# Kernel tuning notes

Measured on AMD Instinct MI355X. Metric: run time of the kernel, lower is better.

## Reference

```python
import jax, jax.numpy as jnp
import numpy as np

B, L, W = 64, 20, 48
D = W * W           # 2304, MoE input/output size (image_width**2)
E = 4               # num_experts
HID = 2 * D         # expert hidden size
K = 1               # top_k
LOSS_COEF = 1e-2


def _cv_squared(x):
    # torch: x.var() (unbiased) / (x.mean()**2 + eps)
    eps = 1e-10
    return jnp.var(x, ddof=1) / (jnp.mean(x) ** 2 + eps)


def _moe(x, w_gate, w1, b1, w2, b2):
    # Noisy top-k gating, inference path (train=False => clean logits, no noise).
    logits = x @ w_gate                                   # [B, E]
    top_logits, top_idx = jax.lax.top_k(logits, K + 1)    # min(k+1, E)
    topk_gates = jax.nn.softmax(top_logits[:, :K], axis=-1)
    gates = jnp.zeros_like(logits).at[
        jnp.arange(x.shape[0])[:, None], top_idx[:, :K]
    ].set(topk_gates)                                     # [B, E] sparse gates
    importance = gates.sum(0)
    load = (gates > 0).sum(0).astype(x.dtype)             # _gates_to_load
    aux = LOSS_COEF * (_cv_squared(importance) + _cv_squared(load))
    # Dense expert compute weighted by gates (same math as dispatch/combine).
    h = jax.nn.relu(jnp.einsum('bd,edh->beh', x, w1) + b1)      # [B,E,HID]
    y = jnp.einsum('beh,ehd->bed', h, w2) + b2                  # [B,E,D]
    out = jnp.einsum('be,bed->bd', gates, y)                    # [B,D]
    return out, aux


def _conv3d(x, w, b, pad):
    y = jax.lax.conv_general_dilated(
        x, w, window_strides=(1, 1, 1), padding=pad,
        dimension_numbers=('NCDHW', 'OIDHW', 'NCDHW'))
    return y + b[None, :, None, None, None]


def _forward(input, conv1_w, conv1_b, conv2_w, conv2_b,
             t_gate, t_w1, t_b1, t_w2, t_b2,
             a_gate, a_w1, a_b1, a_w2, a_b2,
             q_gate, q_w1, q_b1, q_w2, q_b2,
             enc_w, enc_b, dec_w, dec_b):
    x = jnp.transpose(input, (0, 2, 1, 3, 4))                   # [B,1,L,H,W]
    x = jax.nn.relu(_conv3d(x, conv1_w, conv1_b, ((1, 1), (1, 1), (1, 1))))
    x = jax.nn.relu(_conv3d(x, conv2_w, conv2_b, ((0, 0), (1, 1), (1, 1))))  # [B,1,1,H,W]
    xf = x.reshape(x.shape[0], -1)                              # [B, D]
    transform, l1 = _moe(xf, t_gate, t_w1, t_b1, t_w2, t_b2)
    add, l2 = _moe(xf, a_gate, a_w1, a_b1, a_w2, a_b2)
    quad, l3 = _moe(xf, q_gate, q_w1, q_b1, q_w2, q_b2)
    s = input.shape                                             # [B,L,1,H,W]
    transform = transform.reshape(s[0], 1, s[2], s[3], s[4])
    add = add.reshape(s[0], 1, s[2], s[3], s[4])
    quad = quad.reshape(s[0], 1, s[2], s[3], s[4])
    out = input * input * quad + input * transform + add        # [B,L,1,H,W]
    # encoder = Linear(D,D)+ReLU, decoder = Linear(D,D) over flattened H*W
    of = out.reshape(s[0], s[1], D)
    of = jax.nn.relu(of @ enc_w + enc_b)
    of = of @ dec_w + dec_b
    of = jax.nn.sigmoid(of)
    return of.reshape(s), l1 + l2 + l3


def setup_inputs() -> dict:
    key = jax.random.key(0)
    ks = jax.random.split(key, 32)
    sc = 0.02
    inp = {
        'input': jax.random.normal(ks[0], (B, L, 1, W, W), jnp.float32),
        'conv1_w': jax.random.normal(ks[1], (10, 1, 3, 3, 3), jnp.float32) * sc,
        'conv1_b': jnp.zeros((10,), jnp.float32),
        'conv2_w': jax.random.normal(ks[2], (1, 10, L, 3, 3), jnp.float32) * sc,
        'conv2_b': jnp.zeros((1,), jnp.float32),
        'enc_w': jax.random.normal(ks[3], (D, D), jnp.float32) * sc,
        'enc_b': jnp.zeros((D,), jnp.float32),
        'dec_w': jax.random.normal(ks[4], (D, D), jnp.float32) * sc,
        'dec_b': jnp.zeros((D,), jnp.float32),
    }
    for i, p in enumerate(['t', 'a', 'q']):
        k0, k1, k2 = jax.random.split(ks[5 + i], 3)
        inp[p + '_gate'] = jnp.zeros((D, E), jnp.float32) + jax.random.normal(k0, (D, E), jnp.float32) * sc
        inp[p + '_w1'] = jax.random.normal(k1, (E, D, HID), jnp.float32) * sc
        inp[p + '_b1'] = jnp.zeros((E, HID), jnp.float32)
        inp[p + '_w2'] = jax.random.normal(k2, (E, HID, D), jnp.float32) * sc
        inp[p + '_b2'] = jnp.zeros((E, D), jnp.float32)
    return inp


def reference(input, conv1_w, conv1_b, conv2_w, conv2_b,
              t_gate, t_w1, t_b1, t_w2, t_b2,
              a_gate, a_w1, a_b1, a_w2, a_b2,
              q_gate, q_w1, q_b1, q_w2, q_b2,
              enc_w, enc_b, dec_w, dec_b):
    return _forward(input, conv1_w, conv1_b, conv2_w, conv2_b,
                    t_gate, t_w1, t_b1, t_w2, t_b2,
                    a_gate, a_w1, a_b1, a_w2, a_b2,
                    q_gate, q_w1, q_b1, q_w2, q_b2,
                    enc_w, enc_b, dec_w, dec_b)
```

## Files before the change

### kernel.cpp

```cpp
#include <hip/hip_runtime.h>
#include <stdint.h>

#define NB 64
#define NL 20
#define ND 2304
#define NE 4
#define NH 4608
#define NM 1280

typedef float f32x4 __attribute__((ext_vector_type(4)));
typedef __bf16 bf16x8 __attribute__((ext_vector_type(8)));
typedef unsigned short u16;
typedef u16 u16x4 __attribute__((ext_vector_type(4)));
typedef unsigned int u32;
typedef u32 u32x4 __attribute__((ext_vector_type(4)));

__device__ __forceinline__ u16 f2bf(float f) {
  u32 u = __builtin_bit_cast(u32, f);
  u += 0x7fffu + ((u >> 16) & 1u);
  return (u16)(u >> 16);
}

__device__ __forceinline__ void gl_lds16(const void* g, void* l) {
  __builtin_amdgcn_global_load_lds(
      (const __attribute__((address_space(1))) void*)g,
      (__attribute__((address_space(3))) void*)l, 16, 0, 0);
}

#define OFF_XF    147456
#define OFF_H     294912
#define OFF_Y     1179648
#define OFF_AUX   1622016
#define OFF_CNT   1622020
#define OFF_ROWS  1622032
#define OFF_OFB   1622240
#define OFF_H1B   3096800
#define OFF_ENCWB 4571360
#define OFF_DECWB 7225568
#define OFF_XC    9879776
#define OFF_P     10322144

__global__ __launch_bounds__(256) void k_conv(
    const float* __restrict__ in, const float* __restrict__ w1,
    const float* __restrict__ b1, const float* __restrict__ w2,
    float* __restrict__ xfp) {
  __shared__ float insl[3][20][50];
  __shared__ float c1[2][18][50];
  __shared__ float w1s[270];
  __shared__ float w2s[90];
  __shared__ float b1s[10];
  const int d = blockIdx.x, b = blockIdx.y, h = blockIdx.z, t = threadIdx.x;
  const int gy0 = h * 16;
  for (int i = t; i < 270; i += 256) w1s[i] = w1[i];
  for (int i = t; i < 90; i += 256) w2s[i] = w2[(size_t)((i / 9) * 20 + d) * 9 + (i % 9)];
  if (t < 10) b1s[t] = b1[t];
  for (int i = t; i < 3000; i += 256) {
    int s = i / 1000, rr = (i % 1000) / 50, cc = i % 50;
    int gd = d - 1 + s, gy = gy0 - 2 + rr, gx = cc - 1;
    float v = 0.f;
    if (gd >= 0 && gd < NL && (unsigned)gy < 48u && (unsigned)gx < 48u)
      v = in[((size_t)b * NL + gd) * ND + gy * 48 + gx];
    insl[s][rr][cc] = v;
  }
  for (int i = t; i < 1800; i += 256) ((float*)c1)[i] = 0.f;
  float s2[4] = {0.f, 0.f, 0.f, 0.f};
  const int y1 = t / 12, x0 = (t % 12) * 4;
  __syncthreads();
  for (int pc = 0; pc < 5; ++pc) {
    if (t < 216) {
      const int gr = gy0 - 1 + y1;
      if ((unsigned)gr < 48u) {
        float a0[4], a1[4];
        const float bb0 = b1s[2 * pc], bb1 = b1s[2 * pc + 1];
#pragma unroll
        for (int xq = 0; xq < 4; ++xq) { a0[xq] = bb0; a1[xq] = bb1; }
#pragma unroll
        for (int kd = 0; kd < 3; ++kd)
#pragma unroll
          for (int ky = 0; ky < 3; ++ky) {
            float v[6];
#pragma unroll
            for (int i = 0; i < 6; ++i) v[i] = insl[kd][y1 + ky][x0 + i];
            const float* wa = &w1s[(2 * pc) * 27 + kd * 9 + ky * 3];
            const float* wb = wa + 27;
#pragma unroll
            for (int xq = 0; xq < 4; ++xq) {
              a0[xq] += v[xq] * wa[0] + v[xq + 1] * wa[1] + v[xq + 2] * wa[2];
              a1[xq] += v[xq] * wb[0] + v[xq + 1] * wb[1] + v[xq + 2] * wb[2];
            }
          }
#pragma unroll
        for (int xq = 0; xq < 4; ++xq) {
          c1[0][y1][x0 + 1 + xq] = fmaxf(a0[xq], 0.f);
          c1[1][y1][x0 + 1 + xq] = fmaxf(a1[xq], 0.f);
        }
      }
    }
    __syncthreads();
    if (t < 192) {
#pragma unroll
      for (int cc = 0; cc < 2; ++cc) {
#pragma unroll
        for (int ky = 0; ky < 3; ++ky) {
          float v[6];
#pragma unroll
          for (int i = 0; i < 6; ++i) v[i] = c1[cc][y1 + ky][x0 + i];
          const float* wr = &w2s[(2 * pc + cc) * 9 + ky * 3];
#pragma unroll
          for (int xq = 0; xq < 4; ++xq)
            s2[xq] += v[xq] * wr[0] + v[xq + 1] * wr[1] + v[xq + 2] * wr[2];
        }
      }
    }
    __syncthreads();
  }
  if (t < 192) {
    f32x4 o = {s2[0], s2[1], s2[2], s2[3]};
    *(f32x4*)(xfp + ((size_t)d * NB + b) * ND + (gy0 + y1) * 48 + x0) = o;
  }
}

__global__ __launch_bounds__(256) void k_bias_relu(
    const float* __restrict__ xfp, const float* __restrict__ c2b, float* __restrict__ xf) {
  const size_t i = (size_t)blockIdx.x * 256 + threadIdx.x;
  float s = c2b[0];
#pragma unroll
  for (int d = 0; d < NL; ++d) s += xfp[(size_t)d * (NB * ND) + i];
  xf[i] = fmaxf(s, 0.f);
}

__global__ __launch_bounds__(256) void k_gate(
    const float* __restrict__ xf,
    const float* __restrict__ g0, const float* __restrict__ g1, const float* __restrict__ g2,
    float* __restrict__ aux, int* __restrict__ cnt, int* __restrict__ rows) {
  const int p = blockIdx.x, t = threadIdx.x;
  const float* __restrict__ g = (p == 0) ? g0 : ((p == 1) ? g1 : g2);
  __shared__ float lg[64][4];
  __shared__ int lidx[64];
  __shared__ int lcnt[4];
  if (t < 4) lcnt[t] = 0;
  const int wv = t >> 6, l = t & 63;
  for (int b0 = 0; b0 < 64; b0 += 4) {
    int bb = b0 + wv;
    f32x4 acc = {0.f, 0.f, 0.f, 0.f};
    const float* xr = xf + (size_t)bb * ND + l * 36;
    const float* gr = g + (size_t)l * 36 * 4;
#pragma unroll
    for (int i4 = 0; i4 < 9; ++i4) {
      f32x4 xv = *(const f32x4*)(xr + i4 * 4);
#pragma unroll
      for (int qq = 0; qq < 4; ++qq) {
        f32x4 gv = *(const f32x4*)(gr + (i4 * 4 + qq) * 4);
        acc += xv[qq] * gv;
      }
    }
#pragma unroll
    for (int e = 0; e < 4; ++e) {
      float pv = acc[e];
#pragma unroll
      for (int off = 32; off > 0; off >>= 1) pv += __shfl_down(pv, off);
      if (l == 0) lg[bb][e] = pv;
    }
  }
  __syncthreads();
  if (t < 64) {
    float best = lg[t][0];
    int bi = 0;
#pragma unroll
    for (int e = 1; e < 4; ++e)
      if (lg[t][e] > best) { best = lg[t][e]; bi = e; }
    lidx[t] = bi;
    atomicAdd(&lcnt[bi], 1);
  }
  __syncthreads();
  if (t == 0) {
    int ofs[4]; int run = 0;
#pragma unroll
    for (int e = 0; e < 4; ++e) { ofs[e] = run; run += lcnt[e]; cnt[p * 4 + e] = lcnt[e]; }
    for (int b = 0; b < 64; ++b) { int e = lidx[b]; rows[p * 64 + ofs[e]++] = b; }
    float var = 0.f;
#pragma unroll
    for (int e = 0; e < 4; ++e) { float dd = (float)lcnt[e] - 16.f; var += dd * dd; }
    var *= (1.f / 3.f);
    aux[p] = 0.02f * var / (256.f + 1e-10f);
  }
}

__global__ __launch_bounds__(256) void k_gather(
    const float* __restrict__ xf, const int* __restrict__ rows, u16* __restrict__ Xb) {
  const int slot = blockIdx.x, t = threadIdx.x;
  const int r = rows[slot];
  const f32x4* src = (const f32x4*)(xf + (size_t)r * ND);
  u16x4* dst = (u16x4*)(Xb + (size_t)slot * ND);
  for (int i = t; i < ND / 4; i += 256) {
    f32x4 v = src[i];
    u16x4 o;
#pragma unroll
    for (int q = 0; q < 4; ++q) o[q] = f2bf(v[q]);
    dst[i] = o;
  }
}

template <int K, int N, int KS>
__global__ __launch_bounds__(256) void k_moe_mfma(
    const u16* __restrict__ Xb,
    const float* __restrict__ wt, const float* __restrict__ wa, const float* __restrict__ wq,
    const int* __restrict__ cnt, float* __restrict__ P) {
  constexpr int KL = K / KS;
  constexpr int NT = KL / 32;
  const int tile = blockIdx.x;
  const int ks = blockIdx.y;
  const int pe = blockIdx.z >> 1, ch = blockIdx.z & 1;
  const int p = pe >> 2, e = pe & 3;
  const int c = cnt[p * 4 + e];
  const int rstart = ch * 32;
  if (rstart >= c) return;
  const int nrows = min(32, c - rstart);
  int pref = 0;
  for (int e2 = 0; e2 < e; ++e2) pref += cnt[p * 4 + e2];
  const int slot0 = p * 64 + pref + rstart;
  const float* __restrict__ W = (p == 0) ? wt : ((p == 1) ? wa : wq);
  __shared__ float wb[NT][8 * 260];
  const int t = threadIdx.x;
  const int w = t >> 6, l = t & 63;
  const int l15 = l & 15, l4 = l >> 4;
  const int mbase = (w & 1) * 16;
  const int nb0 = (w >> 1) * 32;

  int ar = slot0 + mbase + l15; if (ar > 191) ar = 191;
  const u16* Ag = Xb + (size_t)ar * K + ks * KL + l4 * 8;
  bf16x8 areg[NT];
#pragma unroll
  for (int kt = 0; kt < NT; ++kt) areg[kt] = *(const bf16x8*)(Ag + kt * 32);

  const float* Wg = W + (size_t)e * K * N + (size_t)(ks * KL) * N + tile * 64;
#pragma unroll
  for (int kt = 0; kt < NT; ++kt) {
#pragma unroll
    for (int j = 0; j < 2; ++j)
      gl_lds16(Wg + ((size_t)(kt * 32 + w * 8 + j * 4 + l4)) * N + l15 * 4,
               &wb[kt][(w * 2 + j) * 260]);
  }

  f32x4 acc[2] = {};

#define MOESTEP(KT, VM)                                                       \
  {                                                                           \
    asm volatile("s_waitcnt vmcnt(" #VM ")" ::: "memory");                    \
    __syncthreads();                                                          \
    const float* ww = &wb[KT][0];                                             \
    _Pragma("unroll")                                                         \
    for (int i = 0; i < 2; ++i) {                                             \
      const int nb = nb0 + i * 16 + l15;                                      \
      bf16x8 bfr;                                                             \
      _Pragma("unroll")                                                       \
      for (int jj = 0; jj < 8; ++jj)                                          \
        bfr[jj] = (__bf16)ww[(l4 * 2 + (jj >> 2)) * 260 + (jj & 3) * 64 + nb];\
      acc[i] = __builtin_amdgcn_mfma_f32_16x16x32_bf16(areg[KT], bfr, acc[i], 0, 0, 0); \
    }                                                                         \
  }

  MOESTEP(0, 16); MOESTEP(1, 14); MOESTEP(2, 12); MOESTEP(3, 10);
  MOESTEP(4, 8);  MOESTEP(5, 6);  MOESTEP(6, 4);  MOESTEP(7, 2);
  MOESTEP(8, 0);
#undef MOESTEP

  const size_t pbase = (size_t)ks * 192 * N;
#pragma unroll
  for (int i = 0; i < 2; ++i) {
    const int n = tile * 64 + nb0 + i * 16 + l15;
#pragma unroll
    for (int r = 0; r < 4; ++r) {
      const int m = mbase + l4 * 4 + r;
      if (m < nrows) P[pbase + (size_t)(slot0 + m) * N + n] = acc[i][r];
    }
  }
}

__global__ __launch_bounds__(256) void k_red1(
    const float* __restrict__ P,
    const float* __restrict__ b1t, const float* __restrict__ b1a, const float* __restrict__ b1q,
    const int* __restrict__ cnt, u16* __restrict__ Hb) {
  const int slot = blockIdx.y;
  const int p = slot >> 6, pos = slot & 63;
  int e = 0, run = cnt[p * 4];
  while (pos >= run && e < 3) { ++e; run += cnt[p * 4 + e]; }
  const float* __restrict__ b1 = (p == 0) ? b1t : ((p == 1) ? b1a : b1q);
  const int j0 = blockIdx.x * 1024 + threadIdx.x * 4;
  if (j0 >= NH) return;
  f32x4 s = *(const f32x4*)(b1 + (size_t)e * NH + j0);
#pragma unroll
  for (int ks = 0; ks < 8; ++ks)
    s += *(const f32x4*)(P + ((size_t)ks * 192 + slot) * NH + j0);
  u16x4 o;
#pragma unroll
  for (int q = 0; q < 4; ++q) o[q] = f2bf(fmaxf(s[q], 0.f));
  *(u16x4*)(Hb + (size_t)slot * NH + j0) = o;
}

__global__ __launch_bounds__(256) void k_red2(
    const float* __restrict__ P,
    const float* __restrict__ b2t, const float* __restrict__ b2a, const float* __restrict__ b2q,
    const int* __restrict__ cnt, const int* __restrict__ rows, float* __restrict__ Y) {
  const int slot = blockIdx.y;
  const int p = slot >> 6, pos = slot & 63;
  int e = 0, run = cnt[p * 4];
  while (pos >= run && e < 3) { ++e; run += cnt[p * 4 + e]; }
  const float* __restrict__ b2 = (p == 0) ? b2t : ((p == 1) ? b2a : b2q);
  const int b = rows[slot];
  const int t = threadIdx.x;
  if (t >= 192) return;
  const int j0 = blockIdx.x * 768 + t * 4;
  f32x4 s = *(const f32x4*)(b2 + (size_t)e * ND + j0);
#pragma unroll
  for (int ks = 0; ks < 16; ++ks)
    s += *(const f32x4*)(P + ((size_t)ks * 192 + slot) * ND + j0);
  *(f32x4*)(Y + (size_t)(p * 64 + b) * ND + j0) = s;
}

__global__ __launch_bounds__(256) void k_combine(
    const float* __restrict__ in, const float* __restrict__ Y, u16* __restrict__ ofb) {
  const size_t i = (size_t)blockIdx.x * 256 + threadIdx.x;
  const size_t e0 = i * 4;
  const int row = (int)(e0 / ND);
  const int d = (int)(e0 - (size_t)row * ND);
  const int b = row / NL;
  f32x4 v = *(const f32x4*)(in + e0);
  const size_t yb = (size_t)b * ND + d;
  f32x4 tt = *(const f32x4*)(Y + yb);
  f32x4 aa = *(const f32x4*)(Y + (size_t)64 * ND + yb);
  f32x4 qq = *(const f32x4*)(Y + (size_t)128 * ND + yb);
  u16x4 o;
#pragma unroll
  for (int q = 0; q < 4; ++q) {
    float f = v[q] * v[q] * qq[q] + v[q] * tt[q] + aa[q];
    o[q] = f2bf(f);
  }
  *(u16x4*)(ofb + e0) = o;
}

__global__ __launch_bounds__(256) void k_wt(
    const float* __restrict__ encw, const float* __restrict__ decw,
    u16* __restrict__ encb, u16* __restrict__ decb) {
  __shared__ float tl[32][33];
  const float* __restrict__ src = blockIdx.z ? decw : encw;
  u16* __restrict__ dst = blockIdx.z ? decb : encb;
  const int k0 = blockIdx.x * 32, n0 = blockIdx.y * 32;
  const int tx = threadIdx.x & 31, ty = threadIdx.x >> 5;
  for (int r = ty; r < 32; r += 8) tl[r][tx] = src[(size_t)(k0 + r) * ND + n0 + tx];
  __syncthreads();
  for (int r = ty; r < 32; r += 8) dst[(size_t)(n0 + r) * ND + k0 + tx] = f2bf(tl[tx][r]);
}

template <int MODE>
__global__ __launch_bounds__(256) void k_gemm(
    const u16* __restrict__ A, const u16* __restrict__ Bt,
    const float* __restrict__ bias, void* __restrict__ outp,
    const float* __restrict__ aux) {
  __shared__ u16 As[64 * 32];
  __shared__ u16 Bs[128 * 32];
  const int t = threadIdx.x;
  const int bm = blockIdx.x, bn = blockIdx.y;
  const int lane = t & 63;
  const int wr = (t >> 7) & 1, wc = (t >> 6) & 1;
  const int l15 = lane & 15, l4 = lane >> 4;
  f32x4 acc[2][4] = {};
  const int r0 = t >> 2, kc0 = (t & 3) * 8;
  const int r1 = (t + 256) >> 2, kc1 = ((t + 256) & 3) * 8;
  const size_t baseA = (size_t)(bm * 64) * ND;
  const size_t baseB = (size_t)(bn * 128) * ND;
  for (int k0 = 0; k0 < ND; k0 += 32) {
    *(u32x4*)(As + t * 8) = *(const u32x4*)(A + baseA + (size_t)r0 * ND + k0 + kc0);
    *(u32x4*)(Bs + t * 8) = *(const u32x4*)(Bt + baseB + (size_t)r0 * ND + k0 + kc0);
    *(u32x4*)(Bs + (t + 256) * 8) = *(const u32x4*)(Bt + baseB + (size_t)r1 * ND + k0 + kc1);
    __syncthreads();
    bf16x8 af[2], bfr[4];
#pragma unroll
    for (int i = 0; i < 2; ++i)
      af[i] = *(const bf16x8*)(As + (wr * 32 + i * 16 + l15) * 32 + l4 * 8);
#pragma unroll
    for (int i = 0; i < 4; ++i)
      bfr[i] = *(const bf16x8*)(Bs + (wc * 64 + i * 16 + l15) * 32 + l4 * 8);
#pragma unroll
    for (int mi = 0; mi < 2; ++mi)
#pragma unroll
      for (int ni = 0; ni < 4; ++ni)
        acc[mi][ni] = __builtin_amdgcn_mfma_f32_16x16x32_bf16(af[mi], bfr[ni], acc[mi][ni], 0, 0, 0);
    __syncthreads();
  }
  const int colbase = bn * 128 + wc * 64;
  const int rowbase = bm * 64 + wr * 32;
#pragma unroll
  for (int mi = 0; mi < 2; ++mi) {
#pragma unroll
    for (int ni = 0; ni < 4; ++ni) {
      const int colg = colbase + ni * 16 + l15;
      const float bv = bias[colg];
#pragma unroll
      for (int r = 0; r < 4; ++r) {
        const int rowg = rowbase + mi * 16 + l4 * 4 + r;
        float v = acc[mi][ni][r] + bv;
        if (MODE == 0) {
          ((u16*)outp)[(size_t)rowg * ND + colg] = f2bf(fmaxf(v, 0.f));
        } else {
          ((float*)outp)[(size_t)rowg * ND + colg] = 1.f / (1.f + __expf(-v));
        }
      }
    }
  }
  if (MODE == 1 && bm == 0 && bn == 0 && t == 0)
    ((float*)outp)[(size_t)NM * ND] = aux[0] + aux[1] + aux[2];
}

extern "C" void kernel_launch(void* const* d_in, const int* in_sizes, int n_in,
                              void* d_out, int out_size, void* d_ws, size_t ws_size,
                              hipStream_t stream) {
  (void)in_sizes; (void)n_in; (void)out_size; (void)ws_size;
  const float* input   = (const float*)d_in[0];
  const float* conv1_w = (const float*)d_in[1];
  const float* conv1_b = (const float*)d_in[2];
  const float* conv2_w = (const float*)d_in[3];
  const float* conv2_b = (const float*)d_in[4];
  const float* enc_w   = (const float*)d_in[5];
  const float* enc_b   = (const float*)d_in[6];
  const float* dec_w   = (const float*)d_in[7];
  const float* dec_b   = (const float*)d_in[8];
  const float* gate_t = (const float*)d_in[9];
  const float* w1_t   = (const float*)d_in[10];
  const float* b1_t   = (const float*)d_in[11];
  const float* w2_t   = (const float*)d_in[12];
  const float* b2_t   = (const float*)d_in[13];
  const float* gate_a = (const float*)d_in[14];
  const float* w1_a   = (const float*)d_in[15];
  const float* b1_a   = (const float*)d_in[16];
  const float* w2_a   = (const float*)d_in[17];
  const float* b2_a   = (const float*)d_in[18];
  const float* gate_q = (const float*)d_in[19];
  const float* w1_q   = (const float*)d_in[20];
  const float* b1_q   = (const float*)d_in[21];
  const float* w2_q   = (const float*)d_in[22];
  const float* b2_q   = (const float*)d_in[23];

  float* ws = (float*)d_ws;
  float* xf     = ws + OFF_XF;
  u16*   Hb     = (u16*)(ws + OFF_H);
  float* Y      = ws + OFF_Y;
  float* aux    = ws + OFF_AUX;
  int*   cnt    = (int*)(ws + OFF_CNT);
  int*   rows   = (int*)(ws + OFF_ROWS);
  u16*   ofb    = (u16*)(ws + OFF_OFB);
  u16*   h1b    = (u16*)(ws + OFF_H1B);
  u16*   encwb  = (u16*)(ws + OFF_ENCWB);
  u16*   decwb  = (u16*)(ws + OFF_DECWB);
  u16*   Xcb    = (u16*)(ws + OFF_XC);
  float* P      = ws + OFF_P;

  k_conv<<<dim3(20, 64, 3), 256, 0, stream>>>(input, conv1_w, conv1_b, conv2_w, P);
  k_bias_relu<<<576, 256, 0, stream>>>(P, conv2_b, xf);
  k_wt<<<dim3(72, 72, 2), 256, 0, stream>>>(enc_w, dec_w, encwb, decwb);
  k_gate<<<3, 256, 0, stream>>>(xf, gate_t, gate_a, gate_q, aux, cnt, rows);
  k_gather<<<192, 256, 0, stream>>>(xf, rows, Xcb);
  k_moe_mfma<ND, NH, 8><<<dim3(72, 8, 24), 256, 0, stream>>>(Xcb, w1_t, w1_a, w1_q, cnt, P);
  k_red1<<<dim3(5, 192), 256, 0, stream>>>(P, b1_t, b1_a, b1_q, cnt, Hb);
  k_moe_mfma<NH, ND, 16><<<dim3(36, 16, 24), 256, 0, stream>>>(Hb, w2_t, w2_a, w2_q, cnt, P);
  k_red2<<<dim3(3, 192), 256, 0, stream>>>(P, b2_t, b2_a, b2_q, cnt, rows, Y);
  k_combine<<<2880, 256, 0, stream>>>(input, Y, ofb);
  k_gemm<0><<<dim3(20, 18), 256, 0, stream>>>(ofb, encwb, enc_b, (void*)h1b, aux);
  k_gemm<1><<<dim3(20, 18), 256, 0, stream>>>(h1b, decwb, dec_b, d_out, aux);
}
```

Before: 494.1 us.

## Retile MoE MFMA kernel to 16-row chunks, 256-wide N tiles with double-buffered LDS

Each MoE expert GEMM block now handles 16 token rows and a 256-column weight tile instead of 32 rows and 64 columns. Each wave owns a 64-column slice. Weight staging moves from loading all K slices up front to a two-buffer LDS ring with waitcnt/sync per step. The intent is to cut idle blocks when experts receive few tokens and to shrink LDS footprint for better occupancy, at the cost of extra barriers and a smaller prefetch depth.

```diff
diff --git a/kernel.cpp b/kernel.cpp
--- a/kernel.cpp
+++ b/kernel.cpp
@@ -210,68 +210,68 @@
   constexpr int NT = KL / 32;
   const int tile = blockIdx.x;
   const int ks = blockIdx.y;
-  const int pe = blockIdx.z >> 1, ch = blockIdx.z & 1;
+  const int pe = blockIdx.z >> 2, ch = blockIdx.z & 3;
   const int p = pe >> 2, e = pe & 3;
   const int c = cnt[p * 4 + e];
-  const int rstart = ch * 32;
+  const int rstart = ch * 16;
   if (rstart >= c) return;
-  const int nrows = min(32, c - rstart);
+  const int nrows = min(16, c - rstart);
   int pref = 0;
   for (int e2 = 0; e2 < e; ++e2) pref += cnt[p * 4 + e2];
   const int slot0 = p * 64 + pref + rstart;
   const float* __restrict__ W = (p == 0) ? wt : ((p == 1) ? wa : wq);
-  __shared__ float wb[NT][8 * 260];
+  __shared__ float wb[2][32 * 260 + 24];
   const int t = threadIdx.x;
   const int w = t >> 6, l = t & 63;
   const int l15 = l & 15, l4 = l >> 4;
-  const int mbase = (w & 1) * 16;
-  const int nb0 = (w >> 1) * 32;
-
-  int ar = slot0 + mbase + l15; if (ar > 191) ar = 191;
+
+  int ar = slot0 + l15; if (ar > 191) ar = 191;
   const u16* Ag = Xb + (size_t)ar * K + ks * KL + l4 * 8;
   bf16x8 areg[NT];
 #pragma unroll
   for (int kt = 0; kt < NT; ++kt) areg[kt] = *(const bf16x8*)(Ag + kt * 32);
 
-  const float* Wg = W + (size_t)e * K * N + (size_t)(ks * KL) * N + tile * 64;
-#pragma unroll
-  for (int kt = 0; kt < NT; ++kt) {
-#pragma unroll
-    for (int j = 0; j < 2; ++j)
-      gl_lds16(Wg + ((size_t)(kt * 32 + w * 8 + j * 4 + l4)) * N + l15 * 4,
-               &wb[kt][(w * 2 + j) * 260]);
-  }
-
-  f32x4 acc[2] = {};
-
-#define MOESTEP(KT, VM)                                                       \
-  {                                                                           \
-    asm volatile("s_waitcnt vmcnt(" #VM ")" ::: "memory");                    \
-    __syncthreads();                                                          \
-    const float* ww = &wb[KT][0];                                             \
+  const float* Wg = W + (size_t)e * K * N + (size_t)(ks * KL) * N + tile * 256;
+#define STAGE(BUF, KT)                                                        \
+  { _Pragma("unroll")                                                         \
+    for (int j = 0; j < 8; ++j)                                               \
+      gl_lds16(Wg + (size_t)((KT) * 32 + w * 8 + j) * N + l * 4,              \
+               &wb[BUF][(w * 8 + j) * 260 + w * 8]); }
+
+  f32x4 acc[4] = {};
+
+#define CONSUME(KT)                                                           \
+  { const float* ww = &wb[(KT) & 1][0];                                       \
+    const int kb = l4 * 8 * 260 + l4 * 8 + w * 64 + l15;                      \
     _Pragma("unroll")                                                         \
-    for (int i = 0; i < 2; ++i) {                                             \
-      const int nb = nb0 + i * 16 + l15;                                      \
+    for (int i = 0; i < 4; ++i) {                                             \
       bf16x8 bfr;                                                             \
       _Pragma("unroll")                                                       \
-      for (int jj = 0; jj < 8; ++jj)                                          \
-        bfr[jj] = (__bf16)ww[(l4 * 2 + (jj >> 2)) * 260 + (jj & 3) * 64 + nb];\
+      for (int j = 0; j < 8; ++j) bfr[j] = (__bf16)ww[kb + j * 260 + i * 16]; \
       acc[i] = __builtin_amdgcn_mfma_f32_16x16x32_bf16(areg[KT], bfr, acc[i], 0, 0, 0); \
-    }                                                                         \
-  }
-
-  MOESTEP(0, 16); MOESTEP(1, 14); MOESTEP(2, 12); MOESTEP(3, 10);
-  MOESTEP(4, 8);  MOESTEP(5, 6);  MOESTEP(6, 4);  MOESTEP(7, 2);
-  MOESTEP(8, 0);
-#undef MOESTEP
+    } }
+
+  STAGE(0, 0);
+  STAGE(1, 1);
+#pragma unroll
+  for (int kt = 0; kt < NT; ++kt) {
+    if (kt < NT - 1) { asm volatile("s_waitcnt vmcnt(8)" ::: "memory"); }
+    else             { asm volatile("s_waitcnt vmcnt(0)" ::: "memory"); }
+    __syncthreads();
+    CONSUME(kt);
+    __syncthreads();
+    if (kt + 2 < NT) STAGE(kt & 1, kt + 2);
+  }
+#undef STAGE
+#undef CONSUME
 
   const size_t pbase = (size_t)ks * 192 * N;
 #pragma unroll
-  for (int i = 0; i < 2; ++i) {
-    const int n = tile * 64 + nb0 + i * 16 + l15;
+  for (int i = 0; i < 4; ++i) {
+    const int n = tile * 256 + w * 64 + i * 16 + l15;
 #pragma unroll
     for (int r = 0; r < 4; ++r) {
-      const int m = mbase + l4 * 4 + r;
+      const int m = l4 * 4 + r;
       if (m < nrows) P[pbase + (size_t)(slot0 + m) * N + n] = acc[i][r];
     }
   }
@@ -460,9 +460,9 @@
   k_wt<<<dim3(72, 72, 2), 256, 0, stream>>>(enc_w, dec_w, encwb, decwb);
   k_gate<<<3, 256, 0, stream>>>(xf, gate_t, gate_a, gate_q, aux, cnt, rows);
   k_gather<<<192, 256, 0, stream>>>(xf, rows, Xcb);
-  k_moe_mfma<ND, NH, 8><<<dim3(72, 8, 24), 256, 0, stream>>>(Xcb, w1_t, w1_a, w1_q, cnt, P);
+  k_moe_mfma<ND, NH, 8><<<dim3(18, 8, 48), 256, 0, stream>>>(Xcb, w1_t, w1_a, w1_q, cnt, P);
   k_red1<<<dim3(5, 192), 256, 0, stream>>>(P, b1_t, b1_a, b1_q, cnt, Hb);
-  k_moe_mfma<NH, ND, 16><<<dim3(36, 16, 24), 256, 0, stream>>>(Hb, w2_t, w2_a, w2_q, cnt, P);
+  k_moe_mfma<NH, ND, 16><<<dim3(9, 16, 48), 256, 0, stream>>>(Hb, w2_t, w2_a, w2_q, cnt, P);
   k_red2<<<dim3(3, 192), 256, 0, stream>>>(P, b2_t, b2_a, b2_q, cnt, rows, Y);
   k_combine<<<2880, 256, 0, stream>>>(input, Y, ofb);
   k_gemm<0><<<dim3(20, 18), 256, 0, stream>>>(ofb, encwb, enc_b, (void*)h1b, aux);
```

Result: faster. 481.3 us (median of 2 runs) (-2.6%).
